# Optimization experiments

Measured on AMD Instinct MI355X. Metric: run time of the kernel, lower is better.

## Reference

```python
import jax, jax.numpy as jnp
import numpy as np

T, N, E = 64, 2048, 32768
DIMS = [4, 128, 128, 64, 64]   # input_size, N1, N2, N3, N4
HEADS = 6                      # L attention heads, averaged (concat=False)
HID, N5, NC = 32, 16, 3


def _gat_layer(h, src, dst, ew, W, aS, aD, b, n_nodes, activate):
    # GATConv-style layer with edge weights scaling the attention messages.
    hW = jnp.einsum('nf,fho->nho', h, W)                         # [N,H,out]
    es = jnp.einsum('nho,ho->nh', hW, aS)[src]                   # [E,H]
    ed = jnp.einsum('nho,ho->nh', hW, aD)[dst]                   # [E,H]
    e = jax.nn.leaky_relu(es + ed, 0.2)
    m = jax.ops.segment_max(e, dst, num_segments=n_nodes)       # [N,H]
    m = jnp.where(jnp.isfinite(m), m, 0.0)
    ex = jnp.exp(e - m[dst])
    den = jax.ops.segment_sum(ex, dst, num_segments=n_nodes)
    alpha = ex / (den[dst] + 1e-16)                              # softmax over in-edges
    msg = (alpha * ew[:, None])[:, :, None] * hW[src]            # [E,H,out]
    out = jax.ops.segment_sum(msg, dst, num_segments=n_nodes).mean(axis=1) + b
    return jax.nn.elu(out) if activate else out


def _forward(x1, x2, ei1, ei2, ew1, ew2, xn1, xn2, layers,
             Wih, Whh, bih, bhh, Wc1, bc1, Wc2, bc2, remat=False):
    n_nodes = x1.shape[1]

    def gat_stack(x, src, dst, ew):
        h = x
        for i, (W, aS, aD, b) in enumerate(layers):
            h = _gat_layer(h, src, dst, ew, W, aS, aD, b, n_nodes, i < len(layers) - 1)
        return h                                                 # [N, N4]

    def step(carry, ts):
        x1t, x2t, e1t, e2t, w1t, w2t, n1t, n2t = ts
        g1 = n1t @ gat_stack(x1t, e1t[0], e1t[1], w1t)           # weighted readout [N4]
        g2 = n2t @ gat_stack(x2t, e2t[0], e2t[1], w2t)
        return carry, jnp.concatenate([g1, g2])                  # [2*N4]

    f = jax.checkpoint(step) if remat else step
    _, seq = jax.lax.scan(f, 0, (x1, x2, ei1, ei2, ew1, ew2, xn1, xn2))  # [T, 2*N4]

    def gru_step(h, x):                                          # torch GRU cell math
        gi = Wih @ x + bih
        gh = Whh @ h + bhh
        ir, iz, inn = jnp.split(gi, 3)
        hr, hz, hn = jnp.split(gh, 3)
        r = jax.nn.sigmoid(ir + hr)
        z = jax.nn.sigmoid(iz + hz)
        n = jnp.tanh(inn + r * hn)
        h2 = (1.0 - z) * n + z * h
        return h2, h2

    _, rnn_out = jax.lax.scan(gru_step, jnp.zeros((HID,), x1.dtype), seq)  # [T,HID]
    return jax.nn.relu(rnn_out @ Wc1 + bc1) @ Wc2 + bc2                    # [T,NC]


def setup_inputs() -> dict:
    ks = iter(jax.random.split(jax.random.key(0), 64))
    nk = lambda: next(ks)
    inp = {}
    inp['x1'] = jax.random.normal(nk(), (T, N, DIMS[0]), jnp.float32)
    inp['x2'] = jax.random.normal(nk(), (T, N, DIMS[0]), jnp.float32)
    inp['edge_index1'] = jax.random.randint(nk(), (T, 2, E), 0, N)
    inp['edge_index2'] = jax.random.randint(nk(), (T, 2, E), 0, N)
    inp['edge_weight1'] = jax.random.uniform(nk(), (T, E), jnp.float32)
    inp['edge_weight2'] = jax.random.uniform(nk(), (T, E), jnp.float32)
    inp['x_norm2_1'] = jax.random.uniform(nk(), (T, N), jnp.float32) / N
    inp['x_norm2_2'] = jax.random.uniform(nk(), (T, N), jnp.float32) / N
    inp['window_size'] = T
    for i in range(4):
        fin, fout = DIMS[i], DIMS[i + 1]
        inp[f'W{i}'] = jax.random.normal(nk(), (fin, HEADS, fout), jnp.float32) / np.sqrt(fin)
        inp[f'aS{i}'] = jax.random.normal(nk(), (HEADS, fout), jnp.float32) * 0.1
        inp[f'aD{i}'] = jax.random.normal(nk(), (HEADS, fout), jnp.float32) * 0.1
        inp[f'bg{i}'] = jnp.zeros((fout,), jnp.float32)
    din = 2 * DIMS[4]
    inp['Wih'] = jax.random.normal(nk(), (3 * HID, din), jnp.float32) / np.sqrt(din)
    inp['Whh'] = jax.random.normal(nk(), (3 * HID, HID), jnp.float32) / np.sqrt(HID)
    inp['bih'] = jnp.zeros((3 * HID,), jnp.float32)
    inp['bhh'] = jnp.zeros((3 * HID,), jnp.float32)
    inp['Wc1'] = jax.random.normal(nk(), (HID, N5), jnp.float32) / np.sqrt(HID)
    inp['bc1'] = jnp.zeros((N5,), jnp.float32)
    inp['Wc2'] = jax.random.normal(nk(), (N5, NC), jnp.float32) / np.sqrt(N5)
    inp['bc2'] = jnp.zeros((NC,), jnp.float32)
    return inp


def reference(x1, x2, edge_index1, edge_index2, edge_weight1, edge_weight2,
              x_norm2_1, x_norm2_2, window_size,
              W0, aS0, aD0, bg0, W1, aS1, aD1, bg1,
              W2, aS2, aD2, bg2, W3, aS3, aD3, bg3,
              Wih, Whh, bih, bhh, Wc1, bc1, Wc2, bc2):
    layers = [(W0, aS0, aD0, bg0), (W1, aS1, aD1, bg1),
              (W2, aS2, aD2, bg2), (W3, aS3, aD3, bg3)]
    return _forward(x1, x2, edge_index1, edge_index2, edge_weight1, edge_weight2,
                    x_norm2_1, x_norm2_2, layers,
                    Wih, Whh, bih, bhh, Wc1, bc1, Wc2, bc2)
```

## Files before the change

### kernel.cpp

```cpp
#include <hip/hip_runtime.h>
#include <math.h>

#define TS 64
#define NN 2048
#define NE 32768
#define NH 6
#define NB 128
#define BCAP 6144

typedef __attribute__((ext_vector_type(8))) __bf16 bf16x8;
typedef __attribute__((ext_vector_type(4))) float f32x4;

__device__ __forceinline__ float lrelu(float x){ return x >= 0.0f ? x : 0.2f*x; }
__device__ __forceinline__ float eluf(float x){ return x > 0.0f ? x : expm1f(x); }
__device__ __forceinline__ float sigm(float x){ return 1.0f/(1.0f+expf(-x)); }
__device__ __forceinline__ unsigned short bfhi(float x){ return (unsigned short)(__float_as_uint(x) >> 16); }
__device__ __forceinline__ float bff(unsigned short u){ return __uint_as_float(((unsigned int)u) << 16); }
__device__ __forceinline__ unsigned int packf(float v){
  unsigned short h = bfhi(v);
  unsigned short l = bfhi(v - bff(h));
  return (unsigned int)h | ((unsigned int)l << 16);
}

struct PrepArgs {
// ... 144 lines not shown
void gemm0f_kernel(const float* __restrict__ hx, const float* __restrict__ sdv,
                   const int* __restrict__ row_ptr, const int2* __restrict__ edges,
                   const unsigned short* __restrict__ Bth, const unsigned short* __restrict__ Btl,
                   const float* __restrict__ bias, float* __restrict__ C,
                   int sw, const float* __restrict__ uSn, const float* __restrict__ uDn,
                   float* __restrict__ sdo, int c0) {
  constexpr int BN = 128, K = 24;
  constexpr int STG_B = (2048 + 2048 + BN * 32 + BN * 32) * 2;
  constexpr int EPI_B = (64 * (BN + 1) + 12 * (BN + 1)) * 4;
  constexpr int SMEM_B = STG_B > EPI_B ? STG_B : EPI_B;
  __shared__ __align__(16) char smem[SMEM_B];
  __shared__ float mLs[64 * 6];
  unsigned short* AhL = (unsigned short*)smem;
  unsigned short* AlL = AhL + 2048;
  unsigned short* BhL = AlL + 2048;
  unsigned short* BlL = BhL + BN * 32;
  float* CT = (float*)smem;
  float* uL = CT + 64 * (BN + 1);
  int t = threadIdx.x;
  int lane = t & 63, wv = t >> 6;
  int wm = wv & 1, wc = wv >> 1;
  int l15 = lane & 15, lq = lane >> 4;
  int blk = blockIdx.x;
  const int BPG = NN / 64;
  int m0;
  if (sw) { int xcd = blk & 7, q = blk >> 3; int glx = xcd + ((q / BPG) << 3); int nb = q % BPG; m0 = glx * NN + nb * 64; }
  else    m0 = blk * 64;
  int gl = m0 >> 11, n0 = m0 & (NN - 1);
  int gi = c0 + gl;
  const int* rpg = row_ptr + (size_t)gi * (NN + 1);
  const int2* eg = edges + (size_t)gi * NE;
  const float* sdg = sdv + (size_t)gl * NN * 12;
  const float* hb = hx + (size_t)gl * NN * 4;

  for (int pid = t; pid < 64 * 6; pid += 256) {
    int nl = pid / 6, j = pid - nl * 6;
    int n = n0 + nl;
    int rp = rpg[n], re = rpg[n + 1];
    float d = sdg[n * 12 + 6 + j];
    float m = -INFINITY;
    for (int e = rp; e < re; ++e) m = fmaxf(m, lrelu(sdg[eg[e].x * 12 + j] + d));
    mLs[pid] = m;
  }
  __syncthreads();
  {
    int nl = t >> 2, f = t & 3;
    int n = n0 + nl;
    int rp = rpg[n], re = rpg[n + 1];
    float dj[6], mj[6];
    #pragma unroll
    for (int j = 0; j < 6; ++j) { dj[j] = sdg[n * 12 + 6 + j]; mj[j] = mLs[nl * 6 + j]; }
    float accv[6] = {0.f,0.f,0.f,0.f,0.f,0.f};
    float den[6]  = {0.f,0.f,0.f,0.f,0.f,0.f};
    for (int e = rp; e < re; ++e) {
      int2 p = eg[e];
      float wh = __int_as_float(p.y) * hb[(size_t)p.x * 4 + f];
      const float* srow = sdg + (size_t)p.x * 12;
      #pragma unroll
      for (int j = 0; j < 6; ++j) {
        float ex = expf(lrelu(srow[j] + dj[j]) - mj[j]);
        den[j] += ex;
        accv[j] += ex * wh;
      }
    }
    int s4 = (nl >> 1) & 3;
    #pragma unroll
    for (int j = 0; j < 6; ++j) {
      unsigned int u = packf(accv[j] / (den[j] + 1e-16f));
      int pos = nl * 32 + (((j >> 1) ^ s4) << 3) + ((j & 1) << 2) + f;
      AhL[pos] = (unsigned short)(u & 0xffff);
      AlL[pos] = (unsigned short)(u >> 16);
    }
    #pragma unroll
    for (int j = 6; j < 8; ++j) {
      int pos = nl * 32 + (((j >> 1) ^ s4) << 3) + ((j & 1) << 2) + f;
      AhL[pos] = 0; AlL[pos] = 0;
    }
  }
  #pragma unroll
  for (int i = 0; i < 2; ++i) {
    int q = t + i * 256;
    int n = q >> 2, c = q & 3;
    uint4 vh = make_uint4(0, 0, 0, 0), vl = make_uint4(0, 0, 0, 0);
    int k = c * 8;
    if (k < K) {
      vh = *(const uint4*)(Bth + (size_t)n * K + k);
      vl = *(const uint4*)(Btl + (size_t)n * K + k);
    }
    int pos = n * 32 + ((c ^ ((n >> 1) & 3)) << 3);
    *(uint4*)&BhL[pos] = vh;
    *(uint4*)&BlL[pos] = vl;
  }
  __syncthreads();
  f32x4 acc[2][4];
  #pragma unroll
  for (int i = 0; i < 2; ++i)
    #pragma unroll
    for (int j = 0; j < 4; ++j) { f32x4 z = {0.f,0.f,0.f,0.f}; acc[i][j] = z; }
  bf16x8 ah[2], al[2], bh[4], bl[4];
  #pragma unroll
  for (int fr = 0; fr < 2; ++fr) {
    int row = wm * 32 + fr * 16 + l15;
    int p = row * 32 + ((lq ^ ((row >> 1) & 3)) << 3);
    ah[fr] = *(const bf16x8*)&AhL[p];
    al[fr] = *(const bf16x8*)&AlL[p];
  }
  #pragma unroll
  for (int fc = 0; fc < 4; ++fc) {
    int row = wc * 64 + fc * 16 + l15;
    int p = row * 32 + ((lq ^ ((row >> 1) & 3)) << 3);
    bh[fc] = *(const bf16x8*)&BhL[p];
    bl[fc] = *(const bf16x8*)&BlL[p];
  }
  #pragma unroll
  for (int fr = 0; fr < 2; ++fr)
    #pragma unroll
    for (int fc = 0; fc < 4; ++fc) {
      acc[fr][fc] = __builtin_amdgcn_mfma_f32_16x16x32_bf16(ah[fr], bh[fc], acc[fr][fc], 0, 0, 0);
      acc[fr][fc] = __builtin_amdgcn_mfma_f32_16x16x32_bf16(ah[fr], bl[fc], acc[fr][fc], 0, 0, 0);
      acc[fr][fc] = __builtin_amdgcn_mfma_f32_16x16x32_bf16(al[fr], bh[fc], acc[fr][fc], 0, 0, 0);
    }
  __syncthreads();
  #pragma unroll
  for (int fr = 0; fr < 2; ++fr) {
    int rl0 = wm * 32 + fr * 16 + lq * 4;
    #pragma unroll
    for (int fc = 0; fc < 4; ++fc) {
      int col = wc * 64 + fc * 16 + l15;
      float bv = bias[col];
      #pragma unroll
      for (int r = 0; r < 4; ++r) {
        float v = eluf(acc[fr][fc][r] + bv);
        C[(size_t)(m0 + rl0 + r) * BN + col] = v;
        CT[(rl0 + r) * (BN + 1) + col] = v;
      }
    }
  }
  __syncthreads();
  for (int idx = t; idx < 12 * BN; idx += 256) {
    int j = idx / BN, f = idx - j * BN;
    uL[j * (BN + 1) + f] = (j < 6) ? uSn[j * BN + f] : uDn[(j - 6) * BN + f];
  }
  __syncthreads();
  for (int o = t; o < 64 * 12; o += 256) {
    int rl = o / 12, j = o - rl * 12;
    const float* ur = uL + j * (BN + 1);
    const float* cr = CT + rl * (BN + 1);
    float a = 0.f;
    for (int f = 0; f < BN; ++f) a += cr[f] * ur[f];
    sdo[(size_t)(m0 + rl) * 12 + j] = a;
  }
}

template<int FIN, int PT>
__global__ __launch_bounds__(256)
void aggc_kernel(const float* __restrict__ h, const float* __restrict__ sdv,
                 const int* __restrict__ row_ptr, const int2* __restrict__ edges,
                 unsigned int* __restrict__ agg, int c0, int sw) {
  const int TPN = FIN / 4;
  const int NPB = 256 / TPN;
  const int IL = 4;
  const int BPG = NN / (NPB * IL);
  const int CAP = 80;
  __shared__ float awL[NPB][CAP][6];
  __shared__ int   srcL[NPB][CAP];
  __shared__ float mLs[NPB * 6], ivLs[NPB * 6];
  int t = threadIdx.x, blk = blockIdx.x;
  int gl, nb;
  if (sw) { int xcd = blk & 7, q = blk >> 3; gl = xcd + ((q / BPG) << 3); nb = q % BPG; }
  else    { gl = blk / BPG; nb = blk % BPG; }
  int gi = c0 + gl;
  const int* rpg = row_ptr + (size_t)gi * (NN + 1);
  const int2* eg = edges + (size_t)gi * NE;
  const float* sdg = sdv + (size_t)gl * NN * 12;
  const float4* hb4 = (const float4*)(h + (size_t)gl * NN * FIN);
  unsigned int* aggb = agg + (size_t)gl * NN * (6 * FIN);
  for (int it = 0; it < IL; ++it) {
    __syncthreads();
    int n0 = nb * (NPB * IL) + it * NPB;
    int pid = t / PT, sub = t % PT;
    if (pid < NPB * 6) {
      int nl = pid / 6, j = pid - nl * 6;
      int n = n0 + nl;
      int rp = rpg[n], re = rpg[n + 1];
      float d = sdg[n * 12 + 6 + j];
      float m = -INFINITY;
      for (int e = rp + sub; e < re; e += PT) m = fmaxf(m, lrelu(sdg[eg[e].x * 12 + j] + d));
      #pragma unroll
      for (int msk = PT >> 1; msk; msk >>= 1) m = fmaxf(m, __shfl_xor(m, msk, PT));
      float den = 0.f;
      for (int e = rp + sub; e < re; e += PT) {
        int2 p = eg[e];
        float ex = expf(lrelu(sdg[p.x * 12 + j] + d) - m);
        den += ex;
        int idx = e - rp;
        if (idx < CAP) {
          awL[nl][idx][j] = ex * __int_as_float(p.y);
          if (j == 0) srcL[nl][idx] = p.x;
        }
      }
      #pragma unroll
      for (int msk = PT >> 1; msk; msk >>= 1) den += __shfl_xor(den, msk, PT);
      if (sub == 0) { mLs[pid] = m; ivLs[pid] = 1.f / (den + 1e-16f); }
    }
    __syncthreads();
    int nl = t / TPN, f4 = t % TPN;
    int n = n0 + nl;
    int rp = rpg[n], re = rpg[n + 1];
    float4 acc[6];
    #pragma unroll
    for (int j = 0; j < 6; ++j) acc[j] = make_float4(0.f, 0.f, 0.f, 0.f);
    if (re - rp <= CAP) {
      for (int e = rp; e < re; ++e) {
        int idx = e - rp;
        int sct = srcL[nl][idx];
        float4 hv = hb4[(size_t)sct * TPN + f4];
        #pragma unroll
        for (int j = 0; j < 6; ++j) {
          float a = awL[nl][idx][j];
          acc[j].x += a * hv.x; acc[j].y += a * hv.y;
          acc[j].z += a * hv.z; acc[j].w += a * hv.w;
        }
      }
    } else {
      float dj[6], mj[6];
      #pragma unroll
      for (int j = 0; j < 6; ++j) { dj[j] = sdg[n * 12 + 6 + j]; mj[j] = mLs[nl * 6 + j]; }
      for (int e = rp; e < re; ++e) {
        int idx = e - rp;
        int2 p = eg[e];
        float4 hv = hb4[(size_t)p.x * TPN + f4];
        if (idx < CAP) {
          #pragma unroll
          for (int j = 0; j < 6; ++j) {
            float a = awL[nl][idx][j];
            acc[j].x += a * hv.x; acc[j].y += a * hv.y;
            acc[j].z += a * hv.z; acc[j].w += a * hv.w;
          }
        } else {
          float w = __int_as_float(p.y);
          const float* srow = sdg + (size_t)p.x * 12;
          #pragma unroll
          for (int j = 0; j < 6; ++j) {
            float a = expf(lrelu(srow[j] + dj[j]) - mj[j]) * w;
            acc[j].x += a * hv.x; acc[j].y += a * hv.y;
            acc[j].z += a * hv.z; acc[j].w += a * hv.w;
          }
        }
      }
    }
    unsigned int* ar = aggb + (size_t)n * (6 * FIN);
    #pragma unroll
    for (int j = 0; j < 6; ++j) {
      float iv = ivLs[nl * 6 + j];
      uint4 pk;
      pk.x = packf(acc[j].x * iv); pk.y = packf(acc[j].y * iv);
      pk.z = packf(acc[j].z * iv); pk.w = packf(acc[j].w * iv);
      *(uint4*)(ar + j * FIN + f4 * 4) = pk;
    }
  }
}

template<int BN, int MF, int NF, int WMC, int WCC, int EPI>
__global__ __launch_bounds__(256)
void gemm_mfma_kernel(const unsigned int* __restrict__ A,
                      const unsigned short* __restrict__ Bth,
                      const unsigned short* __restrict__ Btl,
                      const float* __restrict__ bias, float* __restrict__ C,
                      int K, int act, int sw,
                      const float* __restrict__ uSn, const float* __restrict__ uDn,
                      float* __restrict__ sdv,
                      const float* __restrict__ xn1, const float* __restrict__ xn2,
                      float* __restrict__ seqv, int c0) {
  static_assert(BN == WCC * NF * 16 && 64 == WMC * MF * 16, "tile mismatch");
  constexpr int STG_B = (2048 + 2048 + BN * 32 + BN * 32) * 2;
  constexpr int EPI_B = (64 * (BN + 1) + 12 * (BN + 1) + 64 + 256) * 4;
  constexpr int SMEM_B = STG_B > EPI_B ? STG_B : EPI_B;
  __shared__ __align__(16) char smem[SMEM_B];
  unsigned short* AhL = (unsigned short*)smem;
  unsigned short* AlL = AhL + 2048;
  unsigned short* BhL = AlL + 2048;
  unsigned short* BlL = BhL + BN * 32;
  float* CT  = (float*)smem;
  float* uL  = CT + 64 * (BN + 1);
  float* xnL = uL + 12 * (BN + 1);
  float* red = xnL + 64;
  int t = threadIdx.x;
  int lane = t & 63, wv = t >> 6;
  int wm = wv % WMC, wc = wv / WMC;
  int l15 = lane & 15, lq = lane >> 4;
  int blk = blockIdx.x;
  const int BPG = NN / 64;
  int m0;
  if (sw) { int xcd = blk & 7, q = blk >> 3; int gl = xcd + ((q / BPG) << 3); int nb = q % BPG; m0 = gl * NN + nb * 64; }
  else    m0 = blk * 64;
  f32x4 acc[MF][NF];
  #pragma unroll
  for (int i = 0; i < MF; ++i)
    #pragma unroll
    for (int j = 0; j < NF; ++j) { f32x4 z = {0.f, 0.f, 0.f, 0.f}; acc[i][j] = z; }

  for (int k0 = 0; k0 < K; k0 += 32) {
    __syncthreads();
    #pragma unroll
    for (int i = 0; i < 2; ++i) {
      int q = t + i * 256;
      int row = q >> 3, c4 = q & 7;
      uint4 av = make_uint4(0, 0, 0, 0);
      int k = k0 + c4 * 4;
      if (k < K) av = *(const uint4*)(A + (size_t)(m0 + row) * K + k);
      int pos = row * 32 + (((c4 >> 1) ^ ((row >> 1) & 3)) << 3) + ((c4 & 1) << 2);
      *(ushort4*)&AhL[pos] = make_ushort4(av.x & 0xffff, av.y & 0xffff, av.z & 0xffff, av.w & 0xffff);
      *(ushort4*)&AlL[pos] = make_ushort4(av.x >> 16, av.y >> 16, av.z >> 16, av.w >> 16);
    }
    #pragma unroll
    for (int i = 0; i < BN / 64; ++i) {
      int q = t + i * 256;
      int n = q >> 2, c = q & 3;
      uint4 vh = make_uint4(0, 0, 0, 0), vl = make_uint4(0, 0, 0, 0);
      int k = k0 + c * 8;
      if (k < K) {
        vh = *(const uint4*)(Bth + (size_t)n * K + k);
        vl = *(const uint4*)(Btl + (size_t)n * K + k);
      }
      int pos = n * 32 + ((c ^ ((n >> 1) & 3)) << 3);
      *(uint4*)&BhL[pos] = vh;
      *(uint4*)&BlL[pos] = vl;
    }
    __syncthreads();
    bf16x8 ah[MF], al[MF], bh[NF], bl[NF];
    #pragma unroll
    for (int fr = 0; fr < MF; ++fr) {
      int row = wm * MF * 16 + fr * 16 + l15;
      int p = row * 32 + ((lq ^ ((row >> 1) & 3)) << 3);
      ah[fr] = *(const bf16x8*)&AhL[p];
      al[fr] = *(const bf16x8*)&AlL[p];
    }
    #pragma unroll
    for (int fc = 0; fc < NF; ++fc) {
      int row = wc * NF * 16 + fc * 16 + l15;
      int p = row * 32 + ((lq ^ ((row >> 1) & 3)) << 3);
      bh[fc] = *(const bf16x8*)&BhL[p];
      bl[fc] = *(const bf16x8*)&BlL[p];
    }
    #pragma unroll
    for (int fr = 0; fr < MF; ++fr)
      #pragma unroll
      for (int fc = 0; fc < NF; ++fc) {
        acc[fr][fc] = __builtin_amdgcn_mfma_f32_16x16x32_bf16(ah[fr], bh[fc], acc[fr][fc], 0, 0, 0);
        acc[fr][fc] = __builtin_amdgcn_mfma_f32_16x16x32_bf16(ah[fr], bl[fc], acc[fr][fc], 0, 0, 0);
        acc[fr][fc] = __builtin_amdgcn_mfma_f32_16x16x32_bf16(al[fr], bh[fc], acc[fr][fc], 0, 0, 0);
      }
  }
  __syncthreads();
  #pragma unroll
  for (int fr = 0; fr < MF; ++fr) {
    int rl0 = wm * MF * 16 + fr * 16 + lq * 4;
    #pragma unroll
    for (int fc = 0; fc < NF; ++fc) {
      int col = wc * NF * 16 + fc * 16 + l15;
      float bv = bias[col];
      #pragma unroll
      for (int r = 0; r < 4; ++r) {
        float v = acc[fr][fc][r] + bv;
        if (act) v = eluf(v);
        if (EPI != 2) C[(size_t)(m0 + rl0 + r) * BN + col] = v;
        CT[(rl0 + r) * (BN + 1) + col] = v;
      }
    }
  }
  __syncthreads();
  if (EPI == 1) {
    for (int idx = t; idx < 12 * BN; idx += 256) {
      int j = idx / BN, f = idx - j * BN;
      uL[j * (BN + 1) + f] = (j < 6) ? uSn[j * BN + f] : uDn[(j - 6) * BN + f];
    }
    __syncthreads();
    for (int o = t; o < 64 * 12; o += 256) {
      int rl = o / 12, j = o - rl * 12;
      const float* ur = uL + j * (BN + 1);
      const float* cr = CT + rl * (BN + 1);
      float a = 0.f;
      for (int f = 0; f < BN; ++f) a += cr[f] * ur[f];
      sdv[(size_t)(m0 + rl) * 12 + j] = a;
    }
  } else {
    int gl = m0 >> 11;
    int gi = c0 + gl;
    int tt = gi >> 1, ss = gi & 1;
    const float* xn = (ss ? xn2 : xn1) + (size_t)tt * NN;
    int nl0 = m0 & (NN - 1);
    if (t < 64) xnL[t] = xn[nl0 + t];
    __syncthreads();
    int d = t & 63, q = t >> 6;
    float a = 0.f;
    #pragma unroll
    for (int i = 0; i < 16; ++i) a += xnL[q * 16 + i] * CT[(q * 16 + i) * (BN + 1) + d];
    red[t] = a;
    __syncthreads();
    if (t < 64)
      atomicAdd(&seqv[tt * 128 + ss * 64 + t], red[t] + red[t + 64] + red[t + 128] + red[t + 192]);
  }
}

__global__ __launch_bounds__(256)
void gru_head_kernel(const float* __restrict__ seq, const float* __restrict__ Wih,
                     const float* __restrict__ Whh, const float* __restrict__ bih,
                     const float* __restrict__ bhh, const float* __restrict__ Wc1,
                     const float* __restrict__ bc1, const float* __restrict__ Wc2,
                     const float* __restrict__ bc2, float* __restrict__ out) {
  __shared__ float seqs[TS * 128];
  __shared__ float WihT[128 * 96];
  __shared__ float WhhT[32 * 96];
  __shared__ float giAll[TS * 96];
  __shared__ float rnnS[TS * 32];
  __shared__ float Wc1L[32 * 16];
  __shared__ float Wc2L[16 * 3];
  __shared__ float bihL[96], bhhL[96], bc1L[16], bc2L[3];
  __shared__ float ghs[96], hs[32];
  int t = threadIdx.x;
  for (int idx = t; idx < TS * 128; idx += 256) seqs[idx] = seq[idx];
  for (int idx = t; idx < 96 * 128; idx += 256) { int j = idx >> 7, k = idx & 127; WihT[k * 96 + j] = Wih[idx]; }
  for (int idx = t; idx < 96 * 32; idx += 256) { int j = idx >> 5, k = idx & 31; WhhT[k * 96 + j] = Whh[idx]; }
  for (int idx = t; idx < 512; idx += 256) Wc1L[idx] = Wc1[idx];
  if (t < 48) Wc2L[t] = Wc2[t];
  if (t < 96) { bihL[t] = bih[t]; bhhL[t] = bhh[t]; }
  if (t >= 96 && t < 112) bc1L[t - 96] = bc1[t - 96];
  if (t >= 112 && t < 115) bc2L[t - 112] = bc2[t - 112];
  if (t < 32) hs[t] = 0.f;
  __syncthreads();
  for (int o = t; o < TS * 96; o += 256) {
    int tt = o / 96, j = o - tt * 96;
    float a = bihL[j];
    const float* xr = seqs + tt * 128;
    #pragma unroll 4
    for (int k = 0; k < 128; ++k) a += WihT[k * 96 + j] * xr[k];
    giAll[o] = a;
  }
  __syncthreads();
  for (int tt = 0; tt < TS; ++tt) {
    if (t < 96) {
      float b = bhhL[t];
      #pragma unroll
      for (int k = 0; k < 32; ++k) b += WhhT[k * 96 + t] * hs[k];
      ghs[t] = b;
    }
    __syncthreads();
    if (t < 32) {
      const float* gi = giAll + tt * 96;
      float r = sigm(gi[t] + ghs[t]);
      float z = sigm(gi[32 + t] + ghs[32 + t]);
      float nv = tanhf(gi[64 + t] + r * ghs[64 + t]);
      float h2 = (1.f - z) * nv + z * hs[t];
      hs[t] = h2;
      rnnS[tt * 32 + t] = h2;
    }
    __syncthreads();
  }
  for (int o = t; o < TS * 3; o += 256) {
    int tt = o / 3, c = o - tt * 3;
    float accv = bc2L[c];
    #pragma unroll
    for (int m = 0; m < 16; ++m) {
      float hv = bc1L[m];
      #pragma unroll
      for (int k = 0; k < 32; ++k) hv += rnnS[tt * 32 + k] * Wc1L[k * 16 + m];
      hv = fmaxf(hv, 0.f);
      accv += hv * Wc2L[m * 3 + c];
    }
    out[o] = accv;
  }
}

static inline size_t alignup(size_t x) { return (x + 255) & ~(size_t)255; }

extern "C" void kernel_launch(void* const* d_in, const int* in_sizes, int n_in,
                              void* d_out, int out_size, void* d_ws, size_t ws_size,
                              hipStream_t stream) {
  const float* x1  = (const float*)d_in[0];
  const float* x2  = (const float*)d_in[1];
  const int*   ei1 = (const int*)d_in[2];
  const int*   ei2 = (const int*)d_in[3];
  const float* ew1 = (const float*)d_in[4];
  const float* ew2 = (const float*)d_in[5];
  const float* xn1 = (const float*)d_in[6];
  const float* xn2 = (const float*)d_in[7];
  const float* Wih = (const float*)d_in[25];
  const float* Whh = (const float*)d_in[26];
  const float* bih = (const float*)d_in[27];
  const float* bhh = (const float*)d_in[28];
  const float* Wc1 = (const float*)d_in[29];
  const float* bc1 = (const float*)d_in[30];
  const float* Wc2 = (const float*)d_in[31];
  const float* bc2 = (const float*)d_in[32];
  float* out = (float*)d_out;

  const size_t uoffs[4] = {0, 24, 792, 1560};
  const size_t woffs[4] = {0, 3072, 101376, 150528};

  size_t off = 0;
  auto take = [&](size_t bytes) -> size_t { size_t o = off; off += alignup(bytes); return o; };
  size_t o_rowptr = take((size_t)NB * (NN + 1) * sizeof(int));
  size_t o_edges  = take((size_t)NB * NE * sizeof(int2));
  size_t o_uS     = take(1944 * sizeof(float));
  size_t o_uD     = take(1944 * sizeof(float));
  size_t o_bth    = take(175104 * sizeof(unsigned short));
  size_t o_btl    = take(175104 * sizeof(unsigned short));
  size_t o_seq    = take((size_t)TS * 128 * sizeof(float));
  size_t persistent = off;

  const size_t BKT_BYTES = (size_t)NB * 8 * BCAP * sizeof(int2);
  const size_t BKT_NEED  = BKT_BYTES + 4096 + (size_t)NB * NN * sizeof(int);

  int G = 8;
  const int cand[3] = {32, 16, 8};
  for (int ci = 0; ci < 3; ++ci) {
    int g = cand[ci];
    size_t aggB = (size_t)g * NN * 768 * sizeof(unsigned int);
    size_t need = persistent
                + alignup((size_t)g * NN * 4 * sizeof(float))
                + alignup((size_t)g * NN * 128 * sizeof(float))
                + 2 * alignup((size_t)g * NN * 12 * sizeof(float))
                + alignup(aggB > BKT_NEED ? aggB : BKT_NEED);
    if (need <= ws_size) { G = g; break; }
  }
  size_t aggB = (size_t)G * NN * 768 * sizeof(unsigned int);
  size_t o_x   = take((size_t)G * NN * 4 * sizeof(float));
  size_t o_h   = take((size_t)G * NN * 128 * sizeof(float));
  size_t o_sdA = take((size_t)G * NN * 12 * sizeof(float));
  size_t o_sdB = take((size_t)G * NN * 12 * sizeof(float));
  size_t o_agg = take(aggB > BKT_NEED ? aggB : BKT_NEED);
  int sw = ((G & 7) == 0) ? 1 : 0;

  char* ws = (char*)d_ws;
  int*   row_ptr = (int*)(ws + o_rowptr);
  int2*  edges   = (int2*)(ws + o_edges);
  float* uS   = (float*)(ws + o_uS);
  float* uD   = (float*)(ws + o_uD);
  unsigned short* bth = (unsigned short*)(ws + o_bth);
  unsigned short* btl = (unsigned short*)(ws + o_btl);
  float* seq  = (float*)(ws + o_seq);
  float* xbuf = (float*)(ws + o_x);
  float* hbuf = (float*)(ws + o_h);
  float* sdA  = (float*)(ws + o_sdA);
  float* sdB  = (float*)(ws + o_sdB);
  unsigned int* aggbuf = (unsigned int*)(ws + o_agg);
  int2* bkt    = (int2*)(ws + o_agg);
  int*  bktCnt = (int*)(ws + o_agg + BKT_BYTES);
  int*  deg    = (int*)(ws + o_agg + BKT_BYTES + 4096);

  PrepArgs pa;
  for (int l = 0; l < 4; ++l) {
    pa.W[l]  = (const float*)d_in[9 + 4 * l];
    pa.aS[l] = (const float*)d_in[10 + 4 * l];
    pa.aD[l] = (const float*)d_in[11 + 4 * l];
  }
  prep_all_kernel<<<dim3(384, 4), 256, 0, stream>>>(pa, uS, uD, bth, btl);
  hipMemsetAsync(ws + o_agg + BKT_BYTES, 0, 4096 + (size_t)NB * NN * sizeof(int), stream);
  hipMemsetAsync(seq, 0, (size_t)TS * 128 * sizeof(float), stream);
  hist_part_kernel<<<NB * 8, 256, 0, stream>>>(ei1, ei2, deg);
  scan_kernel<<<NB, 256, 0, stream>>>(deg, row_ptr);
  bucketA_kernel<<<NB * 8, 256, 0, stream>>>(ei1, ei2, ew1, ew2, bktCnt, bkt);
  scatterB_kernel<<<NB * 8, 256, 0, stream>>>(bktCnt, bkt, row_ptr, edges);

  for (int c0 = 0; c0 < NB; c0 += G) {
    int rows = G * NN;
    copyx_sd0_kernel<<<rows / 256, 256, 0, stream>>>(x1, x2, uS, uD, xbuf, sdA, c0);

    gemm0f_kernel<<<rows / 64, 256, 0, stream>>>(
        xbuf, sdA, row_ptr, edges, bth + woffs[0], btl + woffs[0],
        (const float*)d_in[12], hbuf, sw, uS + uoffs[1], uD + uoffs[1], sdB, c0);

    aggc_kernel<128, 4><<<rows / 32, 256, 0, stream>>>(hbuf, sdB, row_ptr, edges,
                                                       aggbuf, c0, sw);
    gemm_mfma_kernel<128, 2, 4, 2, 2, 1><<<rows / 64, 256, 0, stream>>>(
        aggbuf, bth + woffs[1], btl + woffs[1], (const float*)d_in[16], hbuf,
        768, 1, sw, uS + uoffs[2], uD + uoffs[2], sdA, nullptr, nullptr, nullptr, c0);

    aggc_kernel<128, 4><<<rows / 32, 256, 0, stream>>>(hbuf, sdA, row_ptr, edges,
                                                       aggbuf, c0, sw);
    gemm_mfma_kernel<64, 1, 4, 4, 1, 1><<<rows / 64, 256, 0, stream>>>(
        aggbuf, bth + woffs[2], btl + woffs[2], (const float*)d_in[20], hbuf,
        768, 1, sw, uS + uoffs[3], uD + uoffs[3], sdB, nullptr, nullptr, nullptr, c0);

    aggc_kernel<64, 2><<<rows / 64, 256, 0, stream>>>(hbuf, sdB, row_ptr, edges,
                                                      aggbuf, c0, sw);
    gemm_mfma_kernel<64, 1, 4, 4, 1, 2><<<rows / 64, 256, 0, stream>>>(
        aggbuf, bth + woffs[3], btl + woffs[3], (const float*)d_in[24], nullptr,
        384, 0, sw, nullptr, nullptr, nullptr, xn1, xn2, seq, c0);
  }

  gru_head_kernel<<<1, 256, 0, stream>>>(seq, Wih, Whh, bih, bhh, Wc1, bc1, Wc2, bc2, out);
}
```

Baseline: 2.702 ms.

## Fuse edge aggregation with MFMA GEMM per layer, keep aggregates in LDS

```diff
diff --git a/kernel.cpp b/kernel.cpp
--- a/kernel.cpp
+++ b/kernel.cpp
@@ -320,36 +320,68 @@
   }
 }
 
-template<int FIN, int PT>
+template<int FIN, int BN, int EPI>
 __global__ __launch_bounds__(256)
-void aggc_kernel(const float* __restrict__ h, const float* __restrict__ sdv,
-                 const int* __restrict__ row_ptr, const int2* __restrict__ edges,
-                 unsigned int* __restrict__ agg, int c0, int sw) {
-  const int TPN = FIN / 4;
-  const int NPB = 256 / TPN;
-  const int IL = 4;
-  const int BPG = NN / (NPB * IL);
-  const int CAP = 80;
-  __shared__ float awL[NPB][CAP][6];
-  __shared__ int   srcL[NPB][CAP];
-  __shared__ float mLs[NPB * 6], ivLs[NPB * 6];
-  int t = threadIdx.x, blk = blockIdx.x;
-  int gl, nb;
-  if (sw) { int xcd = blk & 7, q = blk >> 3; gl = xcd + ((q / BPG) << 3); nb = q % BPG; }
-  else    { gl = blk / BPG; nb = blk % BPG; }
+void fused_layer_kernel(const float* __restrict__ h, const float* __restrict__ sdv,
+                        const int* __restrict__ row_ptr, const int2* __restrict__ edges,
+                        const unsigned short* __restrict__ Bth,
+                        const unsigned short* __restrict__ Btl,
+                        const float* __restrict__ bias, float* __restrict__ C,
+                        int sw, const float* __restrict__ uSn, const float* __restrict__ uDn,
+                        float* __restrict__ sdo,
+                        const float* __restrict__ xn1, const float* __restrict__ xn2,
+                        float* __restrict__ seqv, int c0) {
+  constexpr int K = 6 * FIN;
+  constexpr int BM = 32;
+  constexpr int TPN = FIN / 4;
+  constexpr int BPASS = 256 / TPN;
+  constexpr int NBATCH = BM / BPASS;
+  constexpr int CAP = 80;
+  constexpr int PT = (BPASS * 6 >= 96) ? 2 : 4;
+  constexpr int NF = BN / 32;
+  constexpr int AGG_B = BPASS * CAP * 6 * 4 + BPASS * CAP * 4;
+  constexpr int BSTG_B = BN * 32 * 2 * 2;
+  constexpr int EPI1_B = (BM * (BN + 1) + 12 * (BN + 1)) * 4;
+  constexpr int EPI2_B = BM * (BN + 1) * 4 + 64 * 4 + 256 * 4;
+  constexpr int EPI_B = (EPI == 1) ? EPI1_B : EPI2_B;
+  constexpr int U1 = AGG_B > BSTG_B ? AGG_B : BSTG_B;
+  constexpr int U_B = U1 > EPI_B ? U1 : EPI_B;
+  __shared__ __align__(16) unsigned short AhL[BM * K];
+  __shared__ __align__(16) unsigned short AlL[BM * K];
+  __shared__ __align__(16) char uni[U_B];
+  __shared__ float mLs[BPASS * 6], ivLs[BPASS * 6];
+  float* awL  = (float*)uni;
+  int*   srcL = (int*)(uni + BPASS * CAP * 6 * 4);
+  unsigned short* BhL = (unsigned short*)uni;
+  unsigned short* BlL = BhL + BN * 32;
+  float* CT  = (float*)uni;
+  float* uL  = CT + BM * (BN + 1);
+  float* xnL = CT + BM * (BN + 1);
+  float* red = xnL + 64;
+
+  int t = threadIdx.x;
+  int lane = t & 63, wv = t >> 6;
+  int wm = wv & 1, wc = wv >> 1;
+  int l15 = lane & 15, lq = lane >> 4;
+  int blk = blockIdx.x;
+  constexpr int BPG = NN / BM;
+  int m0;
+  if (sw) { int xcd = blk & 7, q = blk >> 3; int glx = xcd + ((q / BPG) << 3); int nb = q % BPG; m0 = glx * NN + nb * BM; }
+  else    m0 = blk * BM;
+  int gl = m0 >> 11, n0 = m0 & (NN - 1);
   int gi = c0 + gl;
   const int* rpg = row_ptr + (size_t)gi * (NN + 1);
   const int2* eg = edges + (size_t)gi * NE;
   const float* sdg = sdv + (size_t)gl * NN * 12;
   const float4* hb4 = (const float4*)(h + (size_t)gl * NN * FIN);
-  unsigned int* aggb = agg + (size_t)gl * NN * (6 * FIN);
-  for (int it = 0; it < IL; ++it) {
-    __syncthreads();
-    int n0 = nb * (NPB * IL) + it * NPB;
+
+  for (int it = 0; it < NBATCH; ++it) {
+    __syncthreads();
+    int nb0 = n0 + it * BPASS;
     int pid = t / PT, sub = t % PT;
-    if (pid < NPB * 6) {
+    if (pid < BPASS * 6) {
       int nl = pid / 6, j = pid - nl * 6;
-      int n = n0 + nl;
+      int n = nb0 + nl;
       int rp = rpg[n], re = rpg[n + 1];
       float d = sdg[n * 12 + 6 + j];
       float m = -INFINITY;
@@ -363,8 +395,8 @@
         den += ex;
         int idx = e - rp;
         if (idx < CAP) {
-          awL[nl][idx][j] = ex * __int_as_float(p.y);
-          if (j == 0) srcL[nl][idx] = p.x;
+          awL[(nl * CAP + idx) * 6 + j] = ex * __int_as_float(p.y);
+          if (j == 0) srcL[nl * CAP + idx] = p.x;
         }
       }
       #pragma unroll
@@ -373,21 +405,22 @@
     }
     __syncthreads();
     int nl = t / TPN, f4 = t % TPN;
-    int n = n0 + nl;
+    int n = nb0 + nl;
+    int row = it * BPASS + nl;
     int rp = rpg[n], re = rpg[n + 1];
-    float4 acc[6];
-    #pragma unroll
-    for (int j = 0; j < 6; ++j) acc[j] = make_float4(0.f, 0.f, 0.f, 0.f);
+    float4 acc6[6];
+    #pragma unroll
+    for (int j = 0; j < 6; ++j) acc6[j] = make_float4(0.f, 0.f, 0.f, 0.f);
     if (re - rp <= CAP) {
       for (int e = rp; e < re; ++e) {
         int idx = e - rp;
-        int sct = srcL[nl][idx];
+        int sct = srcL[nl * CAP + idx];
         float4 hv = hb4[(size_t)sct * TPN + f4];
         #pragma unroll
         for (int j = 0; j < 6; ++j) {
-          float a = awL[nl][idx][j];
-          acc[j].x += a * hv.x; acc[j].y += a * hv.y;
-          acc[j].z += a * hv.z; acc[j].w += a * hv.w;
+          float a = awL[(nl * CAP + idx) * 6 + j];
+          acc6[j].x += a * hv.x; acc6[j].y += a * hv.y;
+          acc6[j].z += a * hv.z; acc6[j].w += a * hv.w;
         }
       }
     } else {
@@ -401,9 +434,9 @@
         if (idx < CAP) {
           #pragma unroll
           for (int j = 0; j < 6; ++j) {
-            float a = awL[nl][idx][j];
-            acc[j].x += a * hv.x; acc[j].y += a * hv.y;
-            acc[j].z += a * hv.z; acc[j].w += a * hv.w;
+            float a = awL[(nl * CAP + idx) * 6 + j];
+            acc6[j].x += a * hv.x; acc6[j].y += a * hv.y;
+            acc6[j].z += a * hv.z; acc6[j].w += a * hv.w;
           }
         } else {
           float w = __int_as_float(p.y);
@@ -411,130 +444,75 @@
           #pragma unroll
           for (int j = 0; j < 6; ++j) {
             float a = expf(lrelu(srow[j] + dj[j]) - mj[j]) * w;
-            acc[j].x += a * hv.x; acc[j].y += a * hv.y;
-            acc[j].z += a * hv.z; acc[j].w += a * hv.w;
+            acc6[j].x += a * hv.x; acc6[j].y += a * hv.y;
+            acc6[j].z += a * hv.z; acc6[j].w += a * hv.w;
           }
         }
       }
     }
-    unsigned int* ar = aggb + (size_t)n * (6 * FIN);
+    int s4 = (row >> 1) & 3;
     #pragma unroll
     for (int j = 0; j < 6; ++j) {
       float iv = ivLs[nl * 6 + j];
-      uint4 pk;
-      pk.x = packf(acc[j].x * iv); pk.y = packf(acc[j].y * iv);
-      pk.z = packf(acc[j].z * iv); pk.w = packf(acc[j].w * iv);
-      *(uint4*)(ar + j * FIN + f4 * 4) = pk;
-    }
-  }
-}
-
-template<int BN, int MF, int NF, int WMC, int WCC, int EPI>
-__global__ __launch_bounds__(256)
-void gemm_mfma_kernel(const unsigned int* __restrict__ A,
-                      const unsigned short* __restrict__ Bth,
-                      const unsigned short* __restrict__ Btl,
-                      const float* __restrict__ bias, float* __restrict__ C,
-                      int K, int act, int sw,
-                      const float* __restrict__ uSn, const float* __restrict__ uDn,
-                      float* __restrict__ sdv,
-                      const float* __restrict__ xn1, const float* __restrict__ xn2,
-                      float* __restrict__ seqv, int c0) {
-  static_assert(BN == WCC * NF * 16 && 64 == WMC * MF * 16, "tile mismatch");
-  constexpr int STG_B = (2048 + 2048 + BN * 32 + BN * 32) * 2;
-  constexpr int EPI_B = (64 * (BN + 1) + 12 * (BN + 1) + 64 + 256) * 4;
-  constexpr int SMEM_B = STG_B > EPI_B ? STG_B : EPI_B;
-  __shared__ __align__(16) char smem[SMEM_B];
-  unsigned short* AhL = (unsigned short*)smem;
-  unsigned short* AlL = AhL + 2048;
-  unsigned short* BhL = AlL + 2048;
-  unsigned short* BlL = BhL + BN * 32;
-  float* CT  = (float*)smem;
-  float* uL  = CT + 64 * (BN + 1);
-  float* xnL = uL + 12 * (BN + 1);
-  float* red = xnL + 64;
-  int t = threadIdx.x;
-  int lane = t & 63, wv = t >> 6;
-  int wm = wv % WMC, wc = wv / WMC;
-  int l15 = lane & 15, lq = lane >> 4;
-  int blk = blockIdx.x;
-  const int BPG = NN / 64;
-  int m0;
-  if (sw) { int xcd = blk & 7, q = blk >> 3; int gl = xcd + ((q / BPG) << 3); int nb = q % BPG; m0 = gl * NN + nb * 64; }
-  else    m0 = blk * 64;
-  f32x4 acc[MF][NF];
-  #pragma unroll
-  for (int i = 0; i < MF; ++i)
-    #pragma unroll
-    for (int j = 0; j < NF; ++j) { f32x4 z = {0.f, 0.f, 0.f, 0.f}; acc[i][j] = z; }
-
+      unsigned int ux = packf(acc6[j].x * iv), uy = packf(acc6[j].y * iv);
+      unsigned int uz = packf(acc6[j].z * iv), uw = packf(acc6[j].w * iv);
+      int k = j * FIN + f4 * 4;
+      int r32 = k & 31;
+      int pos = row * K + (k & ~31) + ((((r32 >> 3) ^ s4)) << 3) + (r32 & 7);
+      *(ushort4*)&AhL[pos] = make_ushort4(ux & 0xffff, uy & 0xffff, uz & 0xffff, uw & 0xffff);
+      *(ushort4*)&AlL[pos] = make_ushort4(ux >> 16, uy >> 16, uz >> 16, uw >> 16);
+    }
+  }
+
+  f32x4 accf[NF];
+  #pragma unroll
+  for (int j = 0; j < NF; ++j) { f32x4 z = {0.f, 0.f, 0.f, 0.f}; accf[j] = z; }
   for (int k0 = 0; k0 < K; k0 += 32) {
     __syncthreads();
-    #pragma unroll
-    for (int i = 0; i < 2; ++i) {
-      int q = t + i * 256;
-      int row = q >> 3, c4 = q & 7;
-      uint4 av = make_uint4(0, 0, 0, 0);
-      int k = k0 + c4 * 4;
-      if (k < K) av = *(const uint4*)(A + (size_t)(m0 + row) * K + k);
-      int pos = row * 32 + (((c4 >> 1) ^ ((row >> 1) & 3)) << 3) + ((c4 & 1) << 2);
-      *(ushort4*)&AhL[pos] = make_ushort4(av.x & 0xffff, av.y & 0xffff, av.z & 0xffff, av.w & 0xffff);
-      *(ushort4*)&AlL[pos] = make_ushort4(av.x >> 16, av.y >> 16, av.z >> 16, av.w >> 16);
-    }
     #pragma unroll
     for (int i = 0; i < BN / 64; ++i) {
       int q = t + i * 256;
       int n = q >> 2, c = q & 3;
-      uint4 vh = make_uint4(0, 0, 0, 0), vl = make_uint4(0, 0, 0, 0);
-      int k = k0 + c * 8;
-      if (k < K) {
-        vh = *(const uint4*)(Bth + (size_t)n * K + k);
-        vl = *(const uint4*)(Btl + (size_t)n * K + k);
-      }
+      uint4 vh = *(const uint4*)(Bth + (size_t)n * K + k0 + c * 8);
+      uint4 vl = *(const uint4*)(Btl + (size_t)n * K + k0 + c * 8);
       int pos = n * 32 + ((c ^ ((n >> 1) & 3)) << 3);
       *(uint4*)&BhL[pos] = vh;
       *(uint4*)&BlL[pos] = vl;
     }
     __syncthreads();
-    bf16x8 ah[MF], al[MF], bh[NF], bl[NF];
-    #pragma unroll
-    for (int fr = 0; fr < MF; ++fr) {
-      int row = wm * MF * 16 + fr * 16 + l15;
-      int p = row * 32 + ((lq ^ ((row >> 1) & 3)) << 3);
-      ah[fr] = *(const bf16x8*)&AhL[p];
-      al[fr] = *(const bf16x8*)&AlL[p];
-    }
+    int arow = wm * 16 + l15;
+    int ap = arow * K + k0 + ((lq ^ ((arow >> 1) & 3)) << 3);
+    bf16x8 ah = *(const bf16x8*)&AhL[ap];
+    bf16x8 al_ = *(const bf16x8*)&AlL[ap];
+    bf16x8 bh[NF], bl[NF];
     #pragma unroll
     for (int fc = 0; fc < NF; ++fc) {
-      int row = wc * NF * 16 + fc * 16 + l15;
-      int p = row * 32 + ((lq ^ ((row >> 1) & 3)) << 3);
-      bh[fc] = *(const bf16x8*)&BhL[p];
-      bl[fc] = *(const bf16x8*)&BlL[p];
-    }
-    #pragma unroll
-    for (int fr = 0; fr < MF; ++fr)
-      #pragma unroll
-      for (int fc = 0; fc < NF; ++fc) {
-        acc[fr][fc] = __builtin_amdgcn_mfma_f32_16x16x32_bf16(ah[fr], bh[fc], acc[fr][fc], 0, 0, 0);
-        acc[fr][fc] = __builtin_amdgcn_mfma_f32_16x16x32_bf16(ah[fr], bl[fc], acc[fr][fc], 0, 0, 0);
-        acc[fr][fc] = __builtin_amdgcn_mfma_f32_16x16x32_bf16(al[fr], bh[fc], acc[fr][fc], 0, 0, 0);
+      int brow = wc * (NF * 16) + fc * 16 + l15;
+      int bp = brow * 32 + ((lq ^ ((brow >> 1) & 3)) << 3);
+      bh[fc] = *(const bf16x8*)&BhL[bp];
+      bl[fc] = *(const bf16x8*)&BlL[bp];
+    }
+    #pragma unroll
+    for (int fc = 0; fc < NF; ++fc) {
+      accf[fc] = __builtin_amdgcn_mfma_f32_16x16x32_bf16(ah, bh[fc], accf[fc], 0, 0, 0);
+      accf[fc] = __builtin_amdgcn_mfma_f32_16x16x32_bf16(ah, bl[fc], accf[fc], 0, 0, 0);
+      accf[fc] = __builtin_amdgcn_mfma_f32_16x16x32_bf16(al_, bh[fc], accf[fc], 0, 0, 0);
+    }
+  }
+  __syncthreads();
+  int rl0 = wm * 16 + lq * 4;
+  #pragma unroll
+  for (int fc = 0; fc < NF; ++fc) {
+    int col = wc * (NF * 16) + fc * 16 + l15;
+    float bv = bias[col];
+    #pragma unroll
+    for (int r = 0; r < 4; ++r) {
+      float v = accf[fc][r] + bv;
+      if (EPI == 1) {
+        v = eluf(v);
+        C[(size_t)(m0 + rl0 + r) * BN + col] = v;
       }
-  }
-  __syncthreads();
-  #pragma unroll
-  for (int fr = 0; fr < MF; ++fr) {
-    int rl0 = wm * MF * 16 + fr * 16 + lq * 4;
-    #pragma unroll
-    for (int fc = 0; fc < NF; ++fc) {
-      int col = wc * NF * 16 + fc * 16 + l15;
-      float bv = bias[col];
-      #pragma unroll
-      for (int r = 0; r < 4; ++r) {
-        float v = acc[fr][fc][r] + bv;
-        if (act) v = eluf(v);
-        if (EPI != 2) C[(size_t)(m0 + rl0 + r) * BN + col] = v;
-        CT[(rl0 + r) * (BN + 1) + col] = v;
-      }
+      CT[(rl0 + r) * (BN + 1) + col] = v;
     }
   }
   __syncthreads();
@@ -544,78 +522,84 @@
       uL[j * (BN + 1) + f] = (j < 6) ? uSn[j * BN + f] : uDn[(j - 6) * BN + f];
     }
     __syncthreads();
-    for (int o = t; o < 64 * 12; o += 256) {
+    for (int o = t; o < BM * 12; o += 256) {
       int rl = o / 12, j = o - rl * 12;
       const float* ur = uL + j * (BN + 1);
       const float* cr = CT + rl * (BN + 1);
       float a = 0.f;
       for (int f = 0; f < BN; ++f) a += cr[f] * ur[f];
-      sdv[(size_t)(m0 + rl) * 12 + j] = a;
+      sdo[(size_t)(m0 + rl) * 12 + j] = a;
     }
   } else {
-    int gl = m0 >> 11;
-    int gi = c0 + gl;
     int tt = gi >> 1, ss = gi & 1;
     const float* xn = (ss ? xn2 : xn1) + (size_t)tt * NN;
-    int nl0 = m0 & (NN - 1);
-    if (t < 64) xnL[t] = xn[nl0 + t];
-    __syncthreads();
-    int d = t & 63, q = t >> 6;
+    if (t < BM) xnL[t] = xn[n0 + t];
+    __syncthreads();
+    int d = t & 63, q4 = t >> 6;
     float a = 0.f;
     #pragma unroll
-    for (int i = 0; i < 16; ++i) a += xnL[q * 16 + i] * CT[(q * 16 + i) * (BN + 1) + d];
+    for (int i = 0; i < 8; ++i)
+      a += xnL[q4 * 8 + i] * CT[(q4 * 8 + i) * (BN + 1) + d];
     red[t] = a;
     __syncthreads();
     if (t < 64)
-      atomicAdd(&seqv[tt * 128 + ss * 64 + t], red[t] + red[t + 64] + red[t + 128] + red[t + 192]);
-  }
-}
-
-__global__ __launch_bounds__(256)
-void gru_head_kernel(const float* __restrict__ seq, const float* __restrict__ Wih,
-                     const float* __restrict__ Whh, const float* __restrict__ bih,
-                     const float* __restrict__ bhh, const float* __restrict__ Wc1,
-                     const float* __restrict__ bc1, const float* __restrict__ Wc2,
-                     const float* __restrict__ bc2, float* __restrict__ out) {
-  __shared__ float seqs[TS * 128];
-  __shared__ float WihT[128 * 96];
-  __shared__ float WhhT[32 * 96];
-  __shared__ float giAll[TS * 96];
+      atomicAdd(&seqv[tt * 128 + ss * 64 + t],
+                red[t] + red[t + 64] + red[t + 128] + red[t + 192]);
+  }
+}
+
+__global__ __launch_bounds__(128)
+void gi_kernel(const float* __restrict__ seq, const float* __restrict__ Wih,
+               const float* __restrict__ bih, float* __restrict__ giAll) {
+  int o = blockIdx.x * 128 + threadIdx.x;
+  int tt = o / 96, j = o - tt * 96;
+  const float4* wr = (const float4*)(Wih + (size_t)j * 128);
+  const float4* xr = (const float4*)(seq + (size_t)tt * 128);
+  float a = bih[j];
+  #pragma unroll 8
+  for (int k = 0; k < 32; ++k) {
+    float4 w = wr[k], x = xr[k];
+    a += w.x * x.x + w.y * x.y + w.z * x.z + w.w * x.w;
+  }
+  giAll[o] = a;
+}
+
+__global__ __launch_bounds__(128)
+void gru_seq_kernel(const float* __restrict__ giAll, const float* __restrict__ Whh,
+                    const float* __restrict__ bhh, const float* __restrict__ Wc1,
+                    const float* __restrict__ bc1, const float* __restrict__ Wc2,
+                    const float* __restrict__ bc2, float* __restrict__ out) {
+  __shared__ __align__(16) float WhhL[96 * 32];
+  __shared__ __align__(16) float giL[TS * 96];
   __shared__ float rnnS[TS * 32];
-  __shared__ float Wc1L[32 * 16];
-  __shared__ float Wc2L[16 * 3];
-  __shared__ float bihL[96], bhhL[96], bc1L[16], bc2L[3];
-  __shared__ float ghs[96], hs[32];
+  __shared__ float Wc1L[512], Wc2L[48], bc1L[16], bc2L[3], bhhL[96];
+  __shared__ float ghs[96];
+  __shared__ __align__(16) float hs[32];
   int t = threadIdx.x;
-  for (int idx = t; idx < TS * 128; idx += 256) seqs[idx] = seq[idx];
-  for (int idx = t; idx < 96 * 128; idx += 256) { int j = idx >> 7, k = idx & 127; WihT[k * 96 + j] = Wih[idx]; }
-  for (int idx = t; idx < 96 * 32; idx += 256) { int j = idx >> 5, k = idx & 31; WhhT[k * 96 + j] = Whh[idx]; }
-  for (int idx = t; idx < 512; idx += 256) Wc1L[idx] = Wc1[idx];
+  for (int i = t; i < 96 * 32; i += 128) WhhL[i] = Whh[i];
+  for (int i = t; i < TS * 96; i += 128) giL[i] = giAll[i];
+  for (int i = t; i < 512; i += 128) Wc1L[i] = Wc1[i];
   if (t < 48) Wc2L[t] = Wc2[t];
-  if (t < 96) { bihL[t] = bih[t]; bhhL[t] = bhh[t]; }
+  if (t < 96) bhhL[t] = bhh[t];
   if (t >= 96 && t < 112) bc1L[t - 96] = bc1[t - 96];
   if (t >= 112 && t < 115) bc2L[t - 112] = bc2[t - 112];
   if (t < 32) hs[t] = 0.f;
   __syncthreads();
-  for (int o = t; o < TS * 96; o += 256) {
-    int tt = o / 96, j = o - tt * 96;
-    float a = bihL[j];
-    const float* xr = seqs + tt * 128;
-    #pragma unroll 4
-    for (int k = 0; k < 128; ++k) a += WihT[k * 96 + j] * xr[k];
-    giAll[o] = a;
-  }
-  __syncthreads();
   for (int tt = 0; tt < TS; ++tt) {
     if (t < 96) {
+      const float4* wr = (const float4*)(WhhL + t * 32);
+      const float4* hr = (const float4*)hs;
       float b = bhhL[t];
       #pragma unroll
-      for (int k = 0; k < 32; ++k) b += WhhT[k * 96 + t] * hs[k];
+      for (int k = 0; k < 8; ++k) {
+        float4 w = wr[k], x = hr[k];
+        b += w.x * x.x + w.y * x.y + w.z * x.z + w.w * x.w;
+      }
       ghs[t] = b;
     }
     __syncthreads();
     if (t < 32) {
-      const float* gi = giAll + tt * 96;
+      const float* gi = giL + tt * 96;
       float r = sigm(gi[t] + ghs[t]);
       float z = sigm(gi[32 + t] + ghs[32 + t]);
       float nv = tanhf(gi[64 + t] + r * ghs[64 + t]);
@@ -625,7 +609,7 @@
     }
     __syncthreads();
   }
-  for (int o = t; o < TS * 3; o += 256) {
+  for (int o = t; o < TS * 3; o += 128) {
     int tt = o / 3, c = o - tt * 3;
     float accv = bc2L[c];
     #pragma unroll
@@ -641,6 +625,7 @@
 }
 
 static inline size_t alignup(size_t x) { return (x + 255) & ~(size_t)255; }
+static inline size_t maxsz(size_t a, size_t b) { return a > b ? a : b; }
 
 extern "C" void kernel_launch(void* const* d_in, const int* in_sizes, int n_in,
                               void* d_out, int out_size, void* d_ws, size_t ws_size,
@@ -675,29 +660,30 @@
   size_t o_bth    = take(175104 * sizeof(unsigned short));
   size_t o_btl    = take(175104 * sizeof(unsigned short));
   size_t o_seq    = take((size_t)TS * 128 * sizeof(float));
+  size_t o_gi     = take((size_t)TS * 96 * sizeof(float));
   size_t persistent = off;
 
   const size_t BKT_BYTES = (size_t)NB * 8 * BCAP * sizeof(int2);
   const size_t BKT_NEED  = BKT_BYTES + 4096 + (size_t)NB * NN * sizeof(int);
 
   int G = 8;
-  const int cand[3] = {32, 16, 8};
-  for (int ci = 0; ci < 3; ++ci) {
+  const int cand[2] = {16, 8};
+  size_t chunkT = 0;
+  for (int ci = 0; ci < 2; ++ci) {
     int g = cand[ci];
-    size_t aggB = (size_t)g * NN * 768 * sizeof(unsigned int);
-    size_t need = persistent
-                + alignup((size_t)g * NN * 4 * sizeof(float))
-                + alignup((size_t)g * NN * 128 * sizeof(float))
-                + 2 * alignup((size_t)g * NN * 12 * sizeof(float))
-                + alignup(aggB > BKT_NEED ? aggB : BKT_NEED);
-    if (need <= ws_size) { G = g; break; }
-  }
-  size_t aggB = (size_t)G * NN * 768 * sizeof(unsigned int);
-  size_t o_x   = take((size_t)G * NN * 4 * sizeof(float));
-  size_t o_h   = take((size_t)G * NN * 128 * sizeof(float));
-  size_t o_sdA = take((size_t)G * NN * 12 * sizeof(float));
-  size_t o_sdB = take((size_t)G * NN * 12 * sizeof(float));
-  size_t o_agg = take(aggB > BKT_NEED ? aggB : BKT_NEED);
+    size_t ct = alignup((size_t)g * NN * 4 * sizeof(float))
+              + 2 * alignup((size_t)g * NN * 128 * sizeof(float))
+              + 2 * alignup((size_t)g * NN * 12 * sizeof(float));
+    if (persistent + maxsz(ct, BKT_NEED) <= ws_size) { G = g; chunkT = ct; break; }
+    chunkT = ct;
+  }
+  size_t o_big = take(maxsz(chunkT, BKT_NEED));
+  size_t b = o_big;
+  size_t o_x   = b; b += alignup((size_t)G * NN * 4 * sizeof(float));
+  size_t o_hA  = b; b += alignup((size_t)G * NN * 128 * sizeof(float));
+  size_t o_hB  = b; b += alignup((size_t)G * NN * 128 * sizeof(float));
+  size_t o_sdA = b; b += alignup((size_t)G * NN * 12 * sizeof(float));
+  size_t o_sdB = b;
   int sw = ((G & 7) == 0) ? 1 : 0;
 
   char* ws = (char*)d_ws;
@@ -707,15 +693,16 @@
   float* uD   = (float*)(ws + o_uD);
   unsigned short* bth = (unsigned short*)(ws + o_bth);
   unsigned short* btl = (unsigned short*)(ws + o_btl);
-  float* seq  = (float*)(ws + o_seq);
+  float* seq   = (float*)(ws + o_seq);
+  float* giAll = (float*)(ws + o_gi);
   float* xbuf = (float*)(ws + o_x);
-  float* hbuf = (float*)(ws + o_h);
+  float* hA   = (float*)(ws + o_hA);
+  float* hB   = (float*)(ws + o_hB);
   float* sdA  = (float*)(ws + o_sdA);
   float* sdB  = (float*)(ws + o_sdB);
-  unsigned int* aggbuf = (unsigned int*)(ws + o_agg);
-  int2* bkt    = (int2*)(ws + o_agg);
-  int*  bktCnt = (int*)(ws + o_agg + BKT_BYTES);
-  int*  deg    = (int*)(ws + o_agg + BKT_BYTES + 4096);
+  int2* bkt    = (int2*)(ws + o_big);
+  int*  bktCnt = (int*)(ws + o_big + BKT_BYTES);
+  int*  deg    = (int*)(ws + o_big + BKT_BYTES + 4096);
 
   PrepArgs pa;
   for (int l = 0; l < 4; ++l) {
@@ -724,7 +711,7 @@
     pa.aD[l] = (const float*)d_in[11 + 4 * l];
   }
   prep_all_kernel<<<dim3(384, 4), 256, 0, stream>>>(pa, uS, uD, bth, btl);
-  hipMemsetAsync(ws + o_agg + BKT_BYTES, 0, 4096 + (size_t)NB * NN * sizeof(int), stream);
+  hipMemsetAsync(ws + o_big + BKT_BYTES, 0, 4096 + (size_t)NB * NN * sizeof(int), stream);
   hipMemsetAsync(seq, 0, (size_t)TS * 128 * sizeof(float), stream);
   hist_part_kernel<<<NB * 8, 256, 0, stream>>>(ei1, ei2, deg);
   scan_kernel<<<NB, 256, 0, stream>>>(deg, row_ptr);
@@ -737,26 +724,24 @@
 
     gemm0f_kernel<<<rows / 64, 256, 0, stream>>>(
         xbuf, sdA, row_ptr, edges, bth + woffs[0], btl + woffs[0],
-        (const float*)d_in[12], hbuf, sw, uS + uoffs[1], uD + uoffs[1], sdB, c0);
-
-    aggc_kernel<128, 4><<<rows / 32, 256, 0, stream>>>(hbuf, sdB, row_ptr, edges,
-                                                       aggbuf, c0, sw);
-    gemm_mfma_kernel<128, 2, 4, 2, 2, 1><<<rows / 64, 256, 0, stream>>>(
-        aggbuf, bth + woffs[1], btl + woffs[1], (const float*)d_in[16], hbuf,
-        768, 1, sw, uS + uoffs[2], uD + uoffs[2], sdA, nullptr, nullptr, nullptr, c0);
-
-    aggc_kernel<128, 4><<<rows / 32, 256, 0, stream>>>(hbuf, sdA, row_ptr, edges,
-                                                       aggbuf, c0, sw);
-    gemm_mfma_kernel<64, 1, 4, 4, 1, 1><<<rows / 64, 256, 0, stream>>>(
-        aggbuf, bth + woffs[2], btl + woffs[2], (const float*)d_in[20], hbuf,
-        768, 1, sw, uS + uoffs[3], uD + uoffs[3], sdB, nullptr, nullptr, nullptr, c0);
-
-    aggc_kernel<64, 2><<<rows / 64, 256, 0, stream>>>(hbuf, sdB, row_ptr, edges,
-                                                      aggbuf, c0, sw);
-    gemm_mfma_kernel<64, 1, 4, 4, 1, 2><<<rows / 64, 256, 0, stream>>>(
-        aggbuf, bth + woffs[3], btl + woffs[3], (const float*)d_in[24], nullptr,
-        384, 0, sw, nullptr, nullptr, nullptr, xn1, xn2, seq, c0);
-  }
-
-  gru_head_kernel<<<1, 256, 0, stream>>>(seq, Wih, Whh, bih, bhh, Wc1, bc1, Wc2, bc2, out);
-}
+        (const float*)d_in[12], hA, sw, uS + uoffs[1], uD + uoffs[1], sdB, c0);
+
+    fused_layer_kernel<128, 128, 1><<<rows / 32, 256, 0, stream>>>(
+        hA, sdB, row_ptr, edges, bth + woffs[1], btl + woffs[1],
+        (const float*)d_in[16], hB, sw, uS + uoffs[2], uD + uoffs[2], sdA,
+        nullptr, nullptr, nullptr, c0);
+
+    fused_layer_kernel<128, 64, 1><<<rows / 32, 256, 0, stream>>>(
+        hB, sdA, row_ptr, edges, bth + woffs[2], btl + woffs[2],
+        (const float*)d_in[20], hA, sw, uS + uoffs[3], uD + uoffs[3], sdB,
+        nullptr, nullptr, nullptr, c0);
+
+    fused_layer_kernel<64, 64, 2><<<rows / 32, 256, 0, stream>>>(
+        hA, sdB, row_ptr, edges, bth + woffs[3], btl + woffs[3],
+        (const float*)d_in[24], nullptr, sw, nullptr, nullptr, nullptr,
+        xn1, xn2, seq, c0);
+  }
+
+  gi_kernel<<<48, 128, 0, stream>>>(seq, Wih, bih, giAll);
+  gru_seq_kernel<<<1, 128, 0, stream>>>(giAll, Whh, bhh, Wc1, bc1, Wc2, bc2, out);
+}
```

Measured after the change: 3.930 ms. 1.45x slower.
